# Kernel tuning notes

Hardware: AMD Instinct MI355X
Metric: run time of the kernel (lower is better)

The kernel has to match this reference:

```python
import jax, jax.numpy as jnp
import numpy as np

SEQ_LEN = 200
BATCH = 32768
H = 4  # LSTM hidden size


def _lstm_layer(x, Wih, Whh, bih, bhh):
    """PyTorch-semantics LSTM layer. x: [B,T,D] -> [B,T,H]. Gate order i,f,g,o."""
    # precompute input contribution for all timesteps: [B,T,4H]
    xg = jnp.einsum('btd,gd->btg', x, Wih) + bih + bhh

    def step(carry, xt):
        h, c = carry
        g = xt + h @ Whh.T  # [B,4H]
        i, f, gg, o = jnp.split(g, 4, axis=-1)
        c = jax.nn.sigmoid(f) * c + jax.nn.sigmoid(i) * jnp.tanh(gg)
        h = jax.nn.sigmoid(o) * jnp.tanh(c)
        return (h, c), h

    B = x.shape[0]
    z = jnp.zeros((B, Whh.shape[1]), x.dtype)
    _, hs = jax.lax.scan(step, (z, z), jnp.swapaxes(xg, 0, 1))  # [T,B,H]
    return jnp.swapaxes(hs, 0, 1)


def _lstm2(x, Wih0, Whh0, bih0, bhh0, Wih1, Whh1, bih1, bhh1):
    h = _lstm_layer(x, Wih0, Whh0, bih0, bhh0)
    return _lstm_layer(h, Wih1, Whh1, bih1, bhh1)


def setup_inputs() -> dict:
    key = jax.random.key(0)
    ks = iter(jax.random.split(key, 64))
    def p(shape, s=0.1):
        return jax.random.normal(next(ks), shape, jnp.float32) * s
    d = {"x": jax.random.normal(next(ks), (BATCH, 2, SEQ_LEN), jnp.float32)}
    for r in ("r0", "r1"):
        d[f"{r}_Wih0"] = p((4 * H, 1)); d[f"{r}_Whh0"] = p((4 * H, H))
        d[f"{r}_bih0"] = p((4 * H,));  d[f"{r}_bhh0"] = p((4 * H,))
        d[f"{r}_Wih1"] = p((4 * H, H)); d[f"{r}_Whh1"] = p((4 * H, H))
        d[f"{r}_bih1"] = p((4 * H,));  d[f"{r}_bhh1"] = p((4 * H,))
    d["Wp"] = p((40, 2 * SEQ_LEN)); d["bp"] = p((40,))
    d["WH"] = p((128, 4 * SEQ_LEN)); d["bH"] = p((128,))
    d["WL"] = p((128, 4 * SEQ_LEN)); d["bL"] = p((128,))
    d["W1"] = p((80, 256)); d["b1"] = p((80,))
    d["W2"] = p((40, 80)); d["b2"] = p((40,))
    d["W3"] = p((1, 80)); d["b3"] = p((1,))
    return d


def reference(x,
              r0_Wih0, r0_Whh0, r0_bih0, r0_bhh0, r0_Wih1, r0_Whh1, r0_bih1, r0_bhh1,
              r1_Wih0, r1_Whh0, r1_bih0, r1_bhh0, r1_Wih1, r1_Whh1, r1_bih1, r1_bhh1,
              Wp, bp, WH, bH, WL, bL, W1, b1, W2, b2, W3, b3):
    B = x.shape[0]
    x_flat = x.reshape(B, 2 * SEQ_LEN)
    other = x_flat @ Wp.T + bp  # [B,40]

    Hx = x[:, 0, :, None]  # [B,T,1]
    Lx = x[:, 1, :, None]
    Hh = _lstm2(Hx, r0_Wih0, r0_Whh0, r0_bih0, r0_bhh0, r0_Wih1, r0_Whh1, r0_bih1, r0_bhh1)
    Lh = _lstm2(Lx, r1_Wih0, r1_Whh0, r1_bih0, r1_bhh0, r1_Wih1, r1_Whh1, r1_bih1, r1_bhh1)
    Hf = jnp.tanh(Hh.reshape(B, 4 * SEQ_LEN) @ WH.T + bH)  # [B,128]
    Lf = jnp.tanh(Lh.reshape(B, 4 * SEQ_LEN) @ WL.T + bL)
    z = jnp.concatenate([Hf, Lf], axis=1)  # [B,256]
    z = jnp.tanh(z @ W1.T + b1)  # [B,80]
    z = jnp.tanh(z @ W2.T + b2)  # [B,40]
    z = jnp.concatenate([z, other], axis=1)  # [B,80]
    return jax.nn.sigmoid(z @ W3.T + b3)  # [B,1]
```

## Files before the change

kernel.cpp:

```cpp
#include <hip/hip_runtime.h>
#include <hip/hip_bf16.h>

#define BATCH 32768
#define TSEQ 200

typedef __attribute__((ext_vector_type(8))) short short8;
typedef __attribute__((ext_vector_type(4))) float floatx4;
typedef __attribute__((ext_vector_type(2))) float f32x2;

#if __has_builtin(__builtin_amdgcn_exp2f)
__device__ __forceinline__ float EXP2(float x) { return __builtin_amdgcn_exp2f(x); }
#else
__device__ __forceinline__ float EXP2(float x) {
    float r; asm("v_exp_f32 %0, %1" : "=v"(r) : "v"(x)); return r;
}
#endif
__device__ __forceinline__ float RCP(float x) { return __builtin_amdgcn_rcpf(x); }

__device__ __forceinline__ float fast_sigmoid(float x) {
    return RCP(1.0f + EXP2(-1.4426950408889634f * x));
}
__device__ __forceinline__ float fast_tanh(float x) {
    float e = EXP2(2.8853900817779268f * x);
    return 1.0f - 2.0f * RCP(e + 1.0f);
}
__device__ __forceinline__ short f2bfs(float v) {
    __hip_bfloat16 h = __float2bfloat16(v);
    return __builtin_bit_cast(short, h);
}
__device__ __forceinline__ f32x2 splat2(float x) { f32x2 v; v[0] = x; v[1] = x; return v; }
__device__ __forceinline__ f32x2 pkfma(f32x2 a, f32x2 b, f32x2 c) {
    return __builtin_elementwise_fma(a, b, c);
}
template <int K>
__device__ __forceinline__ float qb(float v) {
    int i = __builtin_bit_cast(int, v);
    int r = __builtin_amdgcn_update_dpp(i, i, K * 0x55, 0xf, 0xf, false);
    return __builtin_bit_cast(float, r);
}
__device__ __forceinline__ void async16(void* lds, const void* g) {
    __builtin_amdgcn_global_load_lds(
        (const __attribute__((address_space(1))) unsigned int*)g,
        (__attribute__((address_space(3))) unsigned int*)lds, 16, 0, 0);
}

#define S_SIG (-1.4426950408889634f)
#define S_TANH (2.8853900817779268f)

#define WS_HH  0
#define WS_WHB 104857600
#define WS_WLB (WS_WHB + 204800)
#define WS_W1B (WS_WLB + 204800)
#define WS_W2B (WS_W1B + 40960)
#define WS_U   (WS_W2B + 9216)
#define WS_OT  (WS_U + 1616)
#define WS_Z   (WS_OT + 262144)

struct LW { const float* p[16]; };

__global__ __launch_bounds__(256) void k_prep(
    const float* __restrict__ WH, const float* __restrict__ WL,
    const float* __restrict__ W1, const float* __restrict__ W2,
    const float* __restrict__ W3, const float* __restrict__ Wp,
    const float* __restrict__ bp, const float* __restrict__ b3,
    __hip_bfloat16* __restrict__ WHbf, __hip_bfloat16* __restrict__ WLbf,
    __hip_bfloat16* __restrict__ W1bf, __hip_bfloat16* __restrict__ W2bf,
    float* __restrict__ u)
{
    int gid = blockIdx.x * 256 + threadIdx.x;
    int n = gid / 800, k = gid - n * 800;
    int t = k >> 2, q = k & 3;
    int kp = (t >> 2) * 16 + q * 4 + (t & 3);
    int dst = n * 800 + kp;
    WHbf[dst] = __float2bfloat16(WH[gid]);
    WLbf[dst] = __float2bfloat16(WL[gid]);
    if (gid < 20480) W1bf[gid] = __float2bfloat16(W1[gid]);
    if (gid < 4608) {
        int rr = gid / 96, cc = gid - rr * 96;
        float v = (rr < 40 && cc < 80) ? W2[rr * 80 + cc] : 0.0f;
        W2bf[gid] = __float2bfloat16(v);
    }
    if (gid < 400) {
        float a = 0.f;
        for (int j = 0; j < 40; ++j) a = fmaf(W3[40 + j], Wp[j * 400 + gid], a);
        u[gid] = a;
    } else if (gid == 400) {
        float a = b3[0];
        for (int j = 0; j < 40; ++j) a = fmaf(W3[40 + j], bp[j], a);
        u[400] = a;
    }
}

__global__ __launch_bounds__(256)
__attribute__((amdgpu_waves_per_eu(4, 4))) void k_lstm(
    const float* __restrict__ x, LW w, const float* __restrict__ u,
    __hip_bfloat16* __restrict__ hh, float* __restrict__ otherp)
{
    int gid = blockIdx.x * 256 + threadIdx.x;
    int q = gid & 3;
    int group = gid >> 2;
    int b = group & (BATCH - 1);
    int r = group >> 15;

    const float* Wih0 = w.p[r * 8 + 0];
    const float* Whh0 = w.p[r * 8 + 1];
    const float* bih0 = w.p[r * 8 + 2];
    const float* bhh0 = w.p[r * 8 + 3];
    const float* Wih1 = w.p[r * 8 + 4];
    const float* Whh1 = w.p[r * 8 + 5];
    const float* bih1 = w.p[r * 8 + 6];
    const float* bhh1 = w.p[r * 8 + 7];

    f32x2 wx0p[2], bb0p[2], bb1p[2], whh0p[2][4], wih1p[2][4], whh1p[2][4];
#pragma unroll
    for (int p = 0; p < 2; ++p) {
#pragma unroll
        for (int c = 0; c < 2; ++c) {
            int G = 2 * p + c;
            int j = 4 * G + q;
            float sc = (G == 2) ? S_TANH : S_SIG;
            wx0p[p][c] = Wih0[j] * sc;
            bb0p[p][c] = (bih0[j] + bhh0[j]) * sc;
            bb1p[p][c] = (bih1[j] + bhh1[j]) * sc;
#pragma unroll
            for (int k = 0; k < 4; ++k) {
                whh0p[p][k][c] = Whh0[j * 4 + k] * sc;
                wih1p[p][k][c] = Wih1[j * 4 + k] * sc;
                whh1p[p][k][c] = Whh1[j * 4 + k] * sc;
            }
        }
    }

    const float* xp = x + ((size_t)b * 2 + r) * TSEQ;
    const float* up = u + r * TSEQ;
    __hip_bfloat16* hp = hh + ((size_t)r * BATCH + b) * 800 + q * 4;

    float h0 = 0.f, c0 = 0.f, h1 = 0.f, c1 = 0.f, accO = 0.f;

    for (int tb = 0; tb < TSEQ; tb += 4) {
        float4 xv = *(const float4*)(xp + tb);
        float4 uv = *(const float4*)(up + tb);
        float xa[4] = {xv.x, xv.y, xv.z, xv.w};
        float ua[4] = {uv.x, uv.y, uv.z, uv.w};
        float hb[4];
#pragma unroll
        for (int j = 0; j < 4; ++j) {
            float xt = xa[j];
            accO = fmaf(xt, ua[j], accO);

            float a0 = qb<0>(h0), a1 = qb<1>(h0), a2 = qb<2>(h0), a3 = qb<3>(h0);
            f32x2 g0 = pkfma(splat2(xt), wx0p[0], bb0p[0]);
            f32x2 g1 = pkfma(splat2(xt), wx0p[1], bb0p[1]);
            g0 = pkfma(whh0p[0][0], splat2(a0), g0); g1 = pkfma(whh0p[1][0], splat2(a0), g1);
            g0 = pkfma(whh0p[0][1], splat2(a1), g0); g1 = pkfma(whh0p[1][1], splat2(a1), g1);
            g0 = pkfma(whh0p[0][2], splat2(a2), g0); g1 = pkfma(whh0p[1][2], splat2(a2), g1);
            g0 = pkfma(whh0p[0][3], splat2(a3), g0); g1 = pkfma(whh0p[1][3], splat2(a3), g1);
            float ig = RCP(1.0f + EXP2(g0[0]));
            float fg = RCP(1.0f + EXP2(g0[1]));
            float og = RCP(1.0f + EXP2(g1[1]));
            float tg = 1.0f - 2.0f * RCP(EXP2(g1[0]) + 1.0f);
            c0 = fmaf(fg, c0, ig * tg);
            float th0 = 1.0f - 2.0f * RCP(EXP2(S_TANH * c0) + 1.0f);
            h0 = og * th0;

            float p0 = qb<0>(h0), p1 = qb<1>(h0), p2 = qb<2>(h0), p3 = qb<3>(h0);
            float q0 = qb<0>(h1), q1 = qb<1>(h1), q2 = qb<2>(h1), q3 = qb<3>(h1);
            g0 = bb1p[0]; g1 = bb1p[1];
            g0 = pkfma(wih1p[0][0], splat2(p0), g0); g1 = pkfma(wih1p[1][0], splat2(p0), g1);
            g0 = pkfma(wih1p[0][1], splat2(p1), g0); g1 = pkfma(wih1p[1][1], splat2(p1), g1);
            g0 = pkfma(wih1p[0][2], splat2(p2), g0); g1 = pkfma(wih1p[1][2], splat2(p2), g1);
            g0 = pkfma(wih1p[0][3], splat2(p3), g0); g1 = pkfma(wih1p[1][3], splat2(p3), g1);
            g0 = pkfma(whh1p[0][0], splat2(q0), g0); g1 = pkfma(whh1p[1][0], splat2(q0), g1);
            g0 = pkfma(whh1p[0][1], splat2(q1), g0); g1 = pkfma(whh1p[1][1], splat2(q1), g1);
            g0 = pkfma(whh1p[0][2], splat2(q2), g0); g1 = pkfma(whh1p[1][2], splat2(q2), g1);
            g0 = pkfma(whh1p[0][3], splat2(q3), g0); g1 = pkfma(whh1p[1][3], splat2(q3), g1);
            ig = RCP(1.0f + EXP2(g0[0]));
            fg = RCP(1.0f + EXP2(g0[1]));
            og = RCP(1.0f + EXP2(g1[1]));
            tg = 1.0f - 2.0f * RCP(EXP2(g1[0]) + 1.0f);
            c1 = fmaf(fg, c1, ig * tg);
            float th1 = 1.0f - 2.0f * RCP(EXP2(S_TANH * c1) + 1.0f);
            h1 = og * th1;
            hb[j] = h1;
        }
        ushort4 pk;
        pk.x = (unsigned short)f2bfs(hb[0]);
        pk.y = (unsigned short)f2bfs(hb[1]);
        pk.z = (unsigned short)f2bfs(hb[2]);
        pk.w = (unsigned short)f2bfs(hb[3]);
        *(ushort4*)(hp + tb * 4) = pk;
    }
    if (q == 0) otherp[(size_t)r * BATCH + b] = accO;
}

__global__ __launch_bounds__(256) void k_gemm(
    const __hip_bfloat16* __restrict__ hh,
    const __hip_bfloat16* __restrict__ WHbf, const __hip_bfloat16* __restrict__ WLbf,
    const float* __restrict__ bH, const float* __restrict__ bL,
    __hip_bfloat16* __restrict__ zws)
{
    __shared__ __hip_bfloat16 As[2][128 * 32];
    __shared__ __hip_bfloat16 Bs[2][128 * 32];
    int tid = threadIdx.x;
    int f = blockIdx.y;
    int m0 = blockIdx.x * 128;
    const __hip_bfloat16* A = hh + (size_t)f * BATCH * 800 + (size_t)m0 * 800;
    const __hip_bfloat16* Wb = f ? WLbf : WHbf;
    const float* bias = f ? bL : bH;

    int wv = tid >> 6, lane = tid & 63, l15 = lane & 15, quad = lane >> 4;
    const __hip_bfloat16* ga = A + (size_t)(tid >> 2) * 800 + (tid & 3) * 8;
    const __hip_bfloat16* gb = Wb + (size_t)(tid >> 2) * 800 + (tid & 3) * 8;

    floatx4 acc[2][8] = {};

#define PREFETCH(kc, buf)                                              \
    do {                                                               \
        __hip_bfloat16* la = &As[buf][wv * 512];                       \
        __hip_bfloat16* lb = &Bs[buf][wv * 512];                       \
        async16(la,        ga + (kc) * 32);                            \
        async16(lb,        gb + (kc) * 32);                            \
        async16(la + 2048, ga + 64 * 800 + (kc) * 32);                 \
        async16(lb + 2048, gb + 64 * 800 + (kc) * 32);                 \
    } while (0)

    PREFETCH(0, 0);
    for (int kc = 0; kc < 25; ++kc) {
        __syncthreads();
        if (kc < 24) PREFETCH(kc + 1, (kc + 1) & 1);
        int buf = kc & 1;
        short8 af0 = *(const short8*)(const void*)&As[buf][(wv * 32 + l15) * 32 + quad * 8];
        short8 af1 = *(const short8*)(const void*)&As[buf][(wv * 32 + 16 + l15) * 32 + quad * 8];
#pragma unroll
        for (int nt = 0; nt < 8; ++nt) {
            short8 bfr = *(const short8*)(const void*)&Bs[buf][(nt * 16 + l15) * 32 + quad * 8];
            acc[0][nt] = __builtin_amdgcn_mfma_f32_16x16x32_bf16(af0, bfr, acc[0][nt], 0, 0, 0);
            acc[1][nt] = __builtin_amdgcn_mfma_f32_16x16x32_bf16(af1, bfr, acc[1][nt], 0, 0, 0);
        }
    }
#undef PREFETCH

    float bv[8];
#pragma unroll
    for (int nt = 0; nt < 8; ++nt) bv[nt] = bias[nt * 16 + l15];
#pragma unroll
    for (int mt = 0; mt < 2; ++mt)
#pragma unroll
        for (int nt = 0; nt < 8; ++nt)
#pragma unroll
            for (int rg = 0; rg < 4; ++rg) {
                int row = m0 + wv * 32 + mt * 16 + quad * 4 + rg;
                int col = f * 128 + nt * 16 + l15;
                zws[(size_t)row * 256 + col] =
                    __float2bfloat16(fast_tanh(acc[mt][nt][rg] + bv[nt]));
            }
}

__global__ __launch_bounds__(256) void k_tail(
    const __hip_bfloat16* __restrict__ zws,
    const __hip_bfloat16* __restrict__ W1bf, const __hip_bfloat16* __restrict__ W2bf,
    const float* __restrict__ b1, const float* __restrict__ b2,
    const float* __restrict__ W3, const float* __restrict__ u,
    const float* __restrict__ otherp, float* __restrict__ out)
{
    __shared__ short z1sh[64 * 104];
    __shared__ float z2sh[64 * 49];
    int tid = threadIdx.x;
    int wv = tid >> 6, lane = tid & 63, l15 = lane & 15, quad = lane >> 4;
    int m0 = blockIdx.x * 64;

    for (int i = tid; i < 64 * 24; i += 256) {
        int rr = i / 24, cc = 80 + (i - rr * 24);
        z1sh[rr * 104 + cc] = 0;
    }

    {
        floatx4 acc[5] = {};
#pragma unroll
        for (int kc = 0; kc < 8; ++kc) {
            short8 af = *(const short8*)(const void*)
                (zws + (size_t)(m0 + wv * 16 + l15) * 256 + kc * 32 + quad * 8);
#pragma unroll
            for (int nt = 0; nt < 5; ++nt) {
                short8 bfr = *(const short8*)(const void*)
                    (W1bf + (size_t)(nt * 16 + l15) * 256 + kc * 32 + quad * 8);
                acc[nt] = __builtin_amdgcn_mfma_f32_16x16x32_bf16(af, bfr, acc[nt], 0, 0, 0);
            }
        }
#pragma unroll
        for (int nt = 0; nt < 5; ++nt) {
            int n = nt * 16 + l15;
            float bb = b1[n];
#pragma unroll
            for (int rg = 0; rg < 4; ++rg) {
                int ml = wv * 16 + quad * 4 + rg;
                z1sh[ml * 104 + n] = f2bfs(fast_tanh(acc[nt][rg] + bb));
            }
        }
    }
    __syncthreads();

    {
        floatx4 acc[3] = {};
#pragma unroll
        for (int kc = 0; kc < 3; ++kc) {
            short8 af = *(const short8*)(const void*)
                &z1sh[(wv * 16 + l15) * 104 + kc * 32 + quad * 8];
#pragma unroll
            for (int nt = 0; nt < 3; ++nt) {
                short8 bfr = *(const short8*)(const void*)
                    (W2bf + (size_t)(nt * 16 + l15) * 96 + kc * 32 + quad * 8);
                acc[nt] = __builtin_amdgcn_mfma_f32_16x16x32_bf16(af, bfr, acc[nt], 0, 0, 0);
            }
        }
#pragma unroll
        for (int nt = 0; nt < 3; ++nt) {
            int n = nt * 16 + l15;
            if (n < 40) {
                float bb = b2[n];
#pragma unroll
                for (int rg = 0; rg < 4; ++rg) {
                    int ml = wv * 16 + quad * 4 + rg;
                    z2sh[ml * 49 + n] = fast_tanh(acc[nt][rg] + bb);
                }
            }
        }
    }
    __syncthreads();

    if (tid < 64) {
        int grow = m0 + tid;
        float s = u[400] + otherp[grow] + otherp[BATCH + grow];
        for (int j = 0; j < 40; ++j) s = fmaf(z2sh[tid * 49 + j], W3[j], s);
        out[grow] = fast_sigmoid(s);
    }
}

extern "C" void kernel_launch(void* const* d_in, const int* in_sizes, int n_in,
                              void* d_out, int out_size, void* d_ws, size_t ws_size,
                              hipStream_t stream)
{
    const float* x = (const float*)d_in[0];
    LW w;
    for (int i = 0; i < 16; ++i) w.p[i] = (const float*)d_in[1 + i];
    const float* Wp = (const float*)d_in[17];
    const float* bp = (const float*)d_in[18];
    const float* WH = (const float*)d_in[19];
    const float* bH = (const float*)d_in[20];
    const float* WL = (const float*)d_in[21];
    const float* bL = (const float*)d_in[22];
    const float* W1 = (const float*)d_in[23];
    const float* b1 = (const float*)d_in[24];
    const float* W2 = (const float*)d_in[25];
    const float* b2 = (const float*)d_in[26];
    const float* W3 = (const float*)d_in[27];
    const float* b3 = (const float*)d_in[28];

    char* ws = (char*)d_ws;
    __hip_bfloat16* hh   = (__hip_bfloat16*)(ws + WS_HH);
    __hip_bfloat16* WHbf = (__hip_bfloat16*)(ws + WS_WHB);
    __hip_bfloat16* WLbf = (__hip_bfloat16*)(ws + WS_WLB);
    __hip_bfloat16* W1bf = (__hip_bfloat16*)(ws + WS_W1B);
    __hip_bfloat16* W2bf = (__hip_bfloat16*)(ws + WS_W2B);
    float* u      = (float*)(ws + WS_U);
    float* otherp = (float*)(ws + WS_OT);
    __hip_bfloat16* zws = (__hip_bfloat16*)(ws + WS_Z);
    float* out = (float*)d_out;

    k_prep<<<400, 256, 0, stream>>>(WH, WL, W1, W2, W3, Wp, bp, b3,
                                    WHbf, WLbf, W1bf, W2bf, u);
    k_lstm<<<1024, 256, 0, stream>>>(x, w, u, hh, otherp);
    k_gemm<<<dim3(256, 2), 256, 0, stream>>>(hh, WHbf, WLbf, bH, bL, zws);
    k_tail<<<512, 256, 0, stream>>>(zws, W1bf, W2bf, b1, b2, W3, u, otherp, out);
}
```

Baseline: 337.8 us.

## Fuse LSTM, projection GEMM and MLP tail into one kernel per batch tile

Merges the LSTM, the WH/WL projection GEMM and the small MLP tail into a single kernel. Each block now handles 32 batch rows for both recurrent branches, so the block then runs the projection GEMM over the hidden sequence it just wrote and finishes the MLP in shared memory. This removes two kernel launches and the global round trips for the intermediate z and other-projection buffers. The hidden states still travel through global memory, now read back by the same block, most likely from L2. In exchange each block reloads the full WH/WL weight tiles for only 32 rows, half the waves sit idle in the tail layers, and the larger shared-memory footprint could lower occupancy.

```diff
diff --git a/kernel.cpp b/kernel.cpp
--- a/kernel.cpp
+++ b/kernel.cpp
@@ -53,8 +53,6 @@
 #define WS_W1B (WS_WLB + 204800)
 #define WS_W2B (WS_W1B + 40960)
 #define WS_U   (WS_W2B + 9216)
-#define WS_OT  (WS_U + 1616)
-#define WS_Z   (WS_OT + 262144)
 
 struct LW { const float* p[16]; };
 
@@ -92,15 +90,27 @@
 }
 
 __global__ __launch_bounds__(256)
-__attribute__((amdgpu_waves_per_eu(4, 4))) void k_lstm(
+__attribute__((amdgpu_waves_per_eu(4, 4))) void k_fused(
     const float* __restrict__ x, LW w, const float* __restrict__ u,
-    __hip_bfloat16* __restrict__ hh, float* __restrict__ otherp)
+    __hip_bfloat16* __restrict__ hh,
+    const __hip_bfloat16* __restrict__ WHbf, const __hip_bfloat16* __restrict__ WLbf,
+    const float* __restrict__ bH, const float* __restrict__ bL,
+    const __hip_bfloat16* __restrict__ W1bf, const __hip_bfloat16* __restrict__ W2bf,
+    const float* __restrict__ b1, const float* __restrict__ b2,
+    const float* __restrict__ W3, float* __restrict__ out)
 {
-    int gid = blockIdx.x * 256 + threadIdx.x;
-    int q = gid & 3;
-    int group = gid >> 2;
-    int b = group & (BATCH - 1);
-    int r = group >> 15;
+    __shared__ __align__(16) char smem[33024];
+    short* Bse = (short*)smem;
+    short* zl  = (short*)smem;
+    short* z1l = (short*)(smem + 17024);
+    float* z2l = (float*)(smem + 23808);
+    float* ot  = (float*)(smem + 32768);
+
+    int tid = threadIdx.x;
+    int q = tid & 3;
+    int g = tid >> 2;
+    int r = tid >> 7;
+    int b = blockIdx.x * 32 + (g & 31);
 
     const float* Wih0 = w.p[r * 8 + 0];
     const float* Whh0 = w.p[r * 8 + 1];
@@ -190,101 +200,73 @@
         pk.w = (unsigned short)f2bfs(hb[3]);
         *(ushort4*)(hp + tb * 4) = pk;
     }
-    if (q == 0) otherp[(size_t)r * BATCH + b] = accO;
-}
-
-__global__ __launch_bounds__(256) void k_gemm(
-    const __hip_bfloat16* __restrict__ hh,
-    const __hip_bfloat16* __restrict__ WHbf, const __hip_bfloat16* __restrict__ WLbf,
-    const float* __restrict__ bH, const float* __restrict__ bL,
-    __hip_bfloat16* __restrict__ zws)
-{
-    __shared__ __hip_bfloat16 As[2][128 * 32];
-    __shared__ __hip_bfloat16 Bs[2][128 * 32];
-    int tid = threadIdx.x;
-    int f = blockIdx.y;
-    int m0 = blockIdx.x * 128;
-    const __hip_bfloat16* A = hh + (size_t)f * BATCH * 800 + (size_t)m0 * 800;
-    const __hip_bfloat16* Wb = f ? WLbf : WHbf;
-    const float* bias = f ? bL : bH;
+    if (q == 0) ot[g] = accO;
+    __syncthreads();
 
     int wv = tid >> 6, lane = tid & 63, l15 = lane & 15, quad = lane >> 4;
-    const __hip_bfloat16* ga = A + (size_t)(tid >> 2) * 800 + (tid & 3) * 8;
-    const __hip_bfloat16* gb = Wb + (size_t)(tid >> 2) * 800 + (tid & 3) * 8;
-
-    floatx4 acc[2][8] = {};
-
-#define PREFETCH(kc, buf)                                              \
+    int b0 = blockIdx.x * 32;
+    int f = wv >> 1, mt = wv & 1;
+
+    const __hip_bfloat16* gB0 = WHbf + (size_t)(tid >> 2) * 800 + (tid & 3) * 8;
+    const __hip_bfloat16* gB2 = WLbf + (size_t)(tid >> 2) * 800 + (tid & 3) * 8;
+    const __hip_bfloat16* Ab =
+        hh + ((size_t)f * BATCH + b0 + mt * 16 + l15) * 800 + quad * 8;
+
+#define PF(kc, buf)                                                    \
     do {                                                               \
-        __hip_bfloat16* la = &As[buf][wv * 512];                       \
-        __hip_bfloat16* lb = &Bs[buf][wv * 512];                       \
-        async16(la,        ga + (kc) * 32);                            \
-        async16(lb,        gb + (kc) * 32);                            \
-        async16(la + 2048, ga + 64 * 800 + (kc) * 32);                 \
-        async16(lb + 2048, gb + 64 * 800 + (kc) * 32);                 \
+        char* lb_ = smem + (buf) * 16384 + wv * 1024;                  \
+        async16(lb_,          gB0 + (kc) * 32);                        \
+        async16(lb_ + 4096,   gB0 + 64 * 800 + (kc) * 32);             \
+        async16(lb_ + 8192,   gB2 + (kc) * 32);                        \
+        async16(lb_ + 12288,  gB2 + 64 * 800 + (kc) * 32);             \
     } while (0)
 
-    PREFETCH(0, 0);
+    floatx4 acc[8] = {};
+    short8 af = *(const short8*)(const void*)Ab;
+    PF(0, 0);
     for (int kc = 0; kc < 25; ++kc) {
         __syncthreads();
-        if (kc < 24) PREFETCH(kc + 1, (kc + 1) & 1);
-        int buf = kc & 1;
-        short8 af0 = *(const short8*)(const void*)&As[buf][(wv * 32 + l15) * 32 + quad * 8];
-        short8 af1 = *(const short8*)(const void*)&As[buf][(wv * 32 + 16 + l15) * 32 + quad * 8];
+        short8 afn = af;
+        if (kc < 24) {
+            PF(kc + 1, (kc + 1) & 1);
+            afn = *(const short8*)(const void*)(Ab + (kc + 1) * 32);
+        }
+        const short* Bb = Bse + (kc & 1) * 8192 + f * 4096;
 #pragma unroll
         for (int nt = 0; nt < 8; ++nt) {
-            short8 bfr = *(const short8*)(const void*)&Bs[buf][(nt * 16 + l15) * 32 + quad * 8];
-            acc[0][nt] = __builtin_amdgcn_mfma_f32_16x16x32_bf16(af0, bfr, acc[0][nt], 0, 0, 0);
-            acc[1][nt] = __builtin_amdgcn_mfma_f32_16x16x32_bf16(af1, bfr, acc[1][nt], 0, 0, 0);
-        }
-    }
-#undef PREFETCH
-
-    float bv[8];
-#pragma unroll
-    for (int nt = 0; nt < 8; ++nt) bv[nt] = bias[nt * 16 + l15];
-#pragma unroll
-    for (int mt = 0; mt < 2; ++mt)
-#pragma unroll
-        for (int nt = 0; nt < 8; ++nt)
+            short8 bfr = *(const short8*)(const void*)(Bb + (nt * 16 + l15) * 32 + quad * 8);
+            acc[nt] = __builtin_amdgcn_mfma_f32_16x16x32_bf16(af, bfr, acc[nt], 0, 0, 0);
+        }
+        af = afn;
+    }
+#undef PF
+    __syncthreads();
+
+    {
+        const float* bias = f ? bL : bH;
+#pragma unroll
+        for (int nt = 0; nt < 8; ++nt) {
+            float bb = bias[nt * 16 + l15];
+            int c = f * 128 + nt * 16 + l15;
 #pragma unroll
             for (int rg = 0; rg < 4; ++rg) {
-                int row = m0 + wv * 32 + mt * 16 + quad * 4 + rg;
-                int col = f * 128 + nt * 16 + l15;
-                zws[(size_t)row * 256 + col] =
-                    __float2bfloat16(fast_tanh(acc[mt][nt][rg] + bv[nt]));
-            }
-}
-
-__global__ __launch_bounds__(256) void k_tail(
-    const __hip_bfloat16* __restrict__ zws,
-    const __hip_bfloat16* __restrict__ W1bf, const __hip_bfloat16* __restrict__ W2bf,
-    const float* __restrict__ b1, const float* __restrict__ b2,
-    const float* __restrict__ W3, const float* __restrict__ u,
-    const float* __restrict__ otherp, float* __restrict__ out)
-{
-    __shared__ short z1sh[64 * 104];
-    __shared__ float z2sh[64 * 49];
-    int tid = threadIdx.x;
-    int wv = tid >> 6, lane = tid & 63, l15 = lane & 15, quad = lane >> 4;
-    int m0 = blockIdx.x * 64;
-
-    for (int i = tid; i < 64 * 24; i += 256) {
-        int rr = i / 24, cc = 80 + (i - rr * 24);
-        z1sh[rr * 104 + cc] = 0;
-    }
-
-    {
-        floatx4 acc[5] = {};
-#pragma unroll
+                int m = mt * 16 + quad * 4 + rg;
+                zl[m * 264 + c] = f2bfs(fast_tanh(acc[nt][rg] + bb));
+            }
+        }
+    }
+    __syncthreads();
+
+    if (wv < 2) {
+        floatx4 a1[5] = {};
         for (int kc = 0; kc < 8; ++kc) {
-            short8 af = *(const short8*)(const void*)
-                (zws + (size_t)(m0 + wv * 16 + l15) * 256 + kc * 32 + quad * 8);
+            short8 afz = *(const short8*)(const void*)
+                &zl[(wv * 16 + l15) * 264 + kc * 32 + quad * 8];
 #pragma unroll
             for (int nt = 0; nt < 5; ++nt) {
                 short8 bfr = *(const short8*)(const void*)
                     (W1bf + (size_t)(nt * 16 + l15) * 256 + kc * 32 + quad * 8);
-                acc[nt] = __builtin_amdgcn_mfma_f32_16x16x32_bf16(af, bfr, acc[nt], 0, 0, 0);
+                a1[nt] = __builtin_amdgcn_mfma_f32_16x16x32_bf16(afz, bfr, a1[nt], 0, 0, 0);
             }
         }
 #pragma unroll
@@ -292,25 +274,28 @@
             int n = nt * 16 + l15;
             float bb = b1[n];
 #pragma unroll
-            for (int rg = 0; rg < 4; ++rg) {
-                int ml = wv * 16 + quad * 4 + rg;
-                z1sh[ml * 104 + n] = f2bfs(fast_tanh(acc[nt][rg] + bb));
-            }
-        }
-    }
-    __syncthreads();
-
-    {
-        floatx4 acc[3] = {};
-#pragma unroll
+            for (int rg = 0; rg < 4; ++rg)
+                z1l[(wv * 16 + quad * 4 + rg) * 104 + n] = f2bfs(fast_tanh(a1[nt][rg] + bb));
+        }
+    } else {
+        int i0 = tid - 128;
+        for (int i = i0; i < 512; i += 128) {
+            int rr = i >> 4, cc = 80 + (i & 15);
+            z1l[rr * 104 + cc] = 0;
+        }
+    }
+    __syncthreads();
+
+    if (wv < 2) {
+        floatx4 a2[3] = {};
         for (int kc = 0; kc < 3; ++kc) {
-            short8 af = *(const short8*)(const void*)
-                &z1sh[(wv * 16 + l15) * 104 + kc * 32 + quad * 8];
+            short8 afz = *(const short8*)(const void*)
+                &z1l[(wv * 16 + l15) * 104 + kc * 32 + quad * 8];
 #pragma unroll
             for (int nt = 0; nt < 3; ++nt) {
                 short8 bfr = *(const short8*)(const void*)
                     (W2bf + (size_t)(nt * 16 + l15) * 96 + kc * 32 + quad * 8);
-                acc[nt] = __builtin_amdgcn_mfma_f32_16x16x32_bf16(af, bfr, acc[nt], 0, 0, 0);
+                a2[nt] = __builtin_amdgcn_mfma_f32_16x16x32_bf16(afz, bfr, a2[nt], 0, 0, 0);
             }
         }
 #pragma unroll
@@ -319,20 +304,17 @@
             if (n < 40) {
                 float bb = b2[n];
 #pragma unroll
-                for (int rg = 0; rg < 4; ++rg) {
-                    int ml = wv * 16 + quad * 4 + rg;
-                    z2sh[ml * 49 + n] = fast_tanh(acc[nt][rg] + bb);
-                }
-            }
-        }
-    }
-    __syncthreads();
-
-    if (tid < 64) {
-        int grow = m0 + tid;
-        float s = u[400] + otherp[grow] + otherp[BATCH + grow];
-        for (int j = 0; j < 40; ++j) s = fmaf(z2sh[tid * 49 + j], W3[j], s);
-        out[grow] = fast_sigmoid(s);
+                for (int rg = 0; rg < 4; ++rg)
+                    z2l[(wv * 16 + quad * 4 + rg) * 44 + n] = fast_tanh(a2[nt][rg] + bb);
+            }
+        }
+    }
+    __syncthreads();
+
+    if (tid < 32) {
+        float s = u[400] + ot[tid] + ot[32 + tid];
+        for (int j = 0; j < 40; ++j) s = fmaf(z2l[tid * 44 + j], W3[j], s);
+        out[b0 + tid] = fast_sigmoid(s);
     }
 }
 
@@ -362,14 +344,11 @@
     __hip_bfloat16* WLbf = (__hip_bfloat16*)(ws + WS_WLB);
     __hip_bfloat16* W1bf = (__hip_bfloat16*)(ws + WS_W1B);
     __hip_bfloat16* W2bf = (__hip_bfloat16*)(ws + WS_W2B);
-    float* u      = (float*)(ws + WS_U);
-    float* otherp = (float*)(ws + WS_OT);
-    __hip_bfloat16* zws = (__hip_bfloat16*)(ws + WS_Z);
+    float* u = (float*)(ws + WS_U);
     float* out = (float*)d_out;
 
     k_prep<<<400, 256, 0, stream>>>(WH, WL, W1, W2, W3, Wp, bp, b3,
                                     WHbf, WLbf, W1bf, W2bf, u);
-    k_lstm<<<1024, 256, 0, stream>>>(x, w, u, hh, otherp);
-    k_gemm<<<dim3(256, 2), 256, 0, stream>>>(hh, WHbf, WLbf, bH, bL, zws);
-    k_tail<<<512, 256, 0, stream>>>(zws, W1bf, W2bf, b1, b2, W3, u, otherp, out);
-}
+    k_fused<<<1024, 256, 0, stream>>>(x, w, u, hh, WHbf, WLbf, bH, bL,
+                                      W1bf, W2bf, b1, b2, W3, out);
+}
```

New measurement: 321.3 us. 4.9% less time.
